# Kernel tuning notes

Hardware: AMD Instinct MI355X
Metric: run time of the kernel (lower is better)

Reference implementation:

```python
import jax, jax.numpy as jnp
import numpy as np

B, TQ, TK, DK, DV = 64, 1024, 1024, 64, 64


def setup_inputs() -> dict:
    key = jax.random.key(0)
    kq, kk, kv, km = jax.random.split(key, 4)
    q = jax.random.normal(kq, (B, TQ, DK), dtype=jnp.float32)
    k = jax.random.normal(kk, (B, TK, DK), dtype=jnp.float32)
    v = jax.random.normal(kv, (B, TK, DV), dtype=jnp.float32)
    mask = jax.random.randint(km, (B, TQ, TK), 0, 2).astype(jnp.int32)
    return {"q": q, "k": k, "v": v, "mask": mask}


def reference(q, k, v, mask):
    # attn = q @ k^T / sqrt(d_k)   -> [B, TQ, TK]
    temper = jnp.sqrt(jnp.asarray(q.shape[-1], dtype=jnp.float32))
    attn = jnp.einsum('bqd,bkd->bqk', q, k) / temper
    # mask-add: -1e9 where mask == 0
    mmask = -1e9 * (1.0 - mask.astype(jnp.float32))
    attn = attn + mmask
    attn = jax.nn.softmax(attn, axis=-1)
    # dropout rate is 0.0 -> identity
    out = jnp.einsum('bqk,bkd->bqd', attn, v)
    return (out, attn)
```

## Files before the change

### kernel.cpp

```cpp
#include <hip/hip_runtime.h>
#include <hip/hip_bf16.h>


#define B_   64
#define TQ_  1024
#define TK_  1024
#define DD   64

typedef short short8 __attribute__((ext_vector_type(8)));
typedef float f32x4 __attribute__((ext_vector_type(4)));

#define PSTR 264
#define VSTR 40
#define PWAVE (16 * PSTR)
#define VWAVE (64 * VSTR)

__device__ __forceinline__ unsigned cvt2(float a, float b) {
    __hip_bfloat162 h = __float22bfloat162_rn(make_float2(a, b));
    unsigned u; __builtin_memcpy(&u, &h, 4); return u;
}
__device__ __forceinline__ short cvt1(float a) {
    __hip_bfloat16 h = __float2bfloat16(a);
    short s; __builtin_memcpy(&s, &h, 2); return s;
}

union Frag { short8 s; unsigned u[4]; };

__global__ __launch_bounds__(256, 3) void attn_mfma_kernel(
    const float* __restrict__ qg, const float* __restrict__ kg,
    const float* __restrict__ vg, const int* __restrict__ maskg,
    float* __restrict__ outg, float* __restrict__ attng)
{
    __shared__ __align__(16) short p_lds[4 * PWAVE];
    __shared__ __align__(16) short vt_lds[4 * VWAVE];

    const int t    = threadIdx.x;
    const int wave = t >> 6, lane = t & 63;
    const int quad = lane >> 4, n16 = lane & 15;
    const int b    = blockIdx.y;
    const int q0   = blockIdx.x * 16;
    const int kbase = wave * 256;

    short* pw = p_lds + wave * PWAVE;
    short* vw = vt_lds + wave * VWAVE;
    float* redmax = (float*)vt_lds;
    float* redsum = (float*)vt_lds + 64;

    Frag aq[2];
    {
        const float* qp = qg + ((size_t)(b * TQ_ + q0 + n16)) * DD + quad * 8;
        #pragma unroll
        for (int f = 0; f < 2; ++f) {
            float4 x = *(const float4*)(qp + f * 32);
            float4 y = *(const float4*)(qp + f * 32 + 4);
            aq[f].u[0] = cvt2(x.x, x.y); aq[f].u[1] = cvt2(x.z, x.w);
            aq[f].u[2] = cvt2(y.x, y.y); aq[f].u[3] = cvt2(y.z, y.w);
        }
    }

    float s_reg[64];

    const float* kbp = kg + (size_t)b * TK_ * DD;
    const int*   mbp = maskg + ((size_t)(b * TQ_ + q0 + quad * 4)) * TK_ + kbase + n16;
    #pragma unroll
    for (int kt = 0; kt < 16; ++kt) {
        const int key0 = kbase + kt * 16;
        const float* kp = kbp + (size_t)(key0 + n16) * DD + quad * 8;
        Frag bk[2];
        #pragma unroll
        for (int f = 0; f < 2; ++f) {
            float4 x = *(const float4*)(kp + f * 32);
            float4 y = *(const float4*)(kp + f * 32 + 4);
            bk[f].u[0] = cvt2(x.x, x.y); bk[f].u[1] = cvt2(x.z, x.w);
            bk[f].u[2] = cvt2(y.x, y.y); bk[f].u[3] = cvt2(y.z, y.w);
        }
        f32x4 acc = {0.f, 0.f, 0.f, 0.f};
        acc = __builtin_amdgcn_mfma_f32_16x16x32_bf16(aq[0].s, bk[0].s, acc, 0, 0, 0);
        acc = __builtin_amdgcn_mfma_f32_16x16x32_bf16(aq[1].s, bk[1].s, acc, 0, 0, 0);
        #pragma unroll
        for (int r = 0; r < 4; ++r) {
            const int m = mbp[(size_t)r * TK_ + kt * 16];
            s_reg[kt * 4 + r] = acc[r] * 0.125f + (m ? 0.f : -1e9f);
        }
    }

    float rmax[4];
    #pragma unroll
    for (int r = 0; r < 4; ++r) {
        float m = s_reg[r];
        #pragma unroll
        for (int kt = 1; kt < 16; ++kt) m = fmaxf(m, s_reg[kt * 4 + r]);
        #pragma unroll
        for (int off = 8; off > 0; off >>= 1) m = fmaxf(m, __shfl_xor(m, off));
        rmax[r] = m;
    }
    if (n16 == 0) {
        #pragma unroll
        for (int r = 0; r < 4; ++r) redmax[wave * 16 + quad * 4 + r] = rmax[r];
    }
    __syncthreads();
    float gmax[4];
    #pragma unroll
    for (int r = 0; r < 4; ++r) {
        const int row = quad * 4 + r;
        gmax[r] = fmaxf(fmaxf(redmax[row], redmax[16 + row]),
                        fmaxf(redmax[32 + row], redmax[48 + row]));
    }
    float lsum[4] = {0.f, 0.f, 0.f, 0.f};
    #pragma unroll
    for (int kt = 0; kt < 16; ++kt) {
        #pragma unroll
        for (int r = 0; r < 4; ++r) {
            const float p = __expf(s_reg[kt * 4 + r] - gmax[r]);
            s_reg[kt * 4 + r] = p;
            lsum[r] += p;
        }
    }
    #pragma unroll
    for (int r = 0; r < 4; ++r) {
        #pragma unroll
        for (int off = 8; off > 0; off >>= 1) lsum[r] += __shfl_xor(lsum[r], off);
    }
    if (n16 == 0) {
        #pragma unroll
        for (int r = 0; r < 4; ++r) redsum[wave * 16 + quad * 4 + r] = lsum[r];
    }
    __syncthreads();
    float inv[4];
    #pragma unroll
    for (int r = 0; r < 4; ++r) {
        const int row = quad * 4 + r;
        inv[r] = 1.f / (redsum[row] + redsum[16 + row] + redsum[32 + row] + redsum[48 + row]);
    }
    __syncthreads();

    float* abp = attng + ((size_t)(b * TQ_ + q0 + quad * 4)) * TK_ + kbase + n16;
    #pragma unroll
    for (int kt = 0; kt < 16; ++kt) {
        #pragma unroll
        for (int r = 0; r < 4; ++r) {
            const float pv = s_reg[kt * 4 + r] * inv[r];
            abp[(size_t)r * TK_ + kt * 16] = pv;
            pw[(quad * 4 + r) * PSTR + kt * 16 + n16] = cvt1(pv);
        }
    }

    f32x4 oacc[4];
    #pragma unroll
    for (int dg = 0; dg < 4; ++dg) oacc[dg] = (f32x4){0.f, 0.f, 0.f, 0.f};

    const float* vbp = vg + (size_t)b * TK_ * DD;
    #pragma unroll 1
    for (int c = 0; c < 8; ++c) {
        const int ck0 = kbase + c * 32;
        #pragma unroll
        for (int i = 0; i < 16; ++i) {
            const float v0 = vbp[(size_t)(ck0 + 2 * i) * DD + lane];
            const float v1 = vbp[(size_t)(ck0 + 2 * i + 1) * DD + lane];
            *(unsigned*)(vw + lane * VSTR + 2 * i) = cvt2(v0, v1);
        }
        Frag pf;
        pf.s = *(const short8*)(pw + n16 * PSTR + c * 32 + quad * 8);
        #pragma unroll
        for (int dg = 0; dg < 4; ++dg) {
            Frag vf;
            vf.s = *(const short8*)(vw + (dg * 16 + n16) * VSTR + quad * 8);
            oacc[dg] = __builtin_amdgcn_mfma_f32_16x16x32_bf16(pf.s, vf.s, oacc[dg], 0, 0, 0);
        }
    }

    float* ow = (float*)pw;
    #pragma unroll
    for (int dg = 0; dg < 4; ++dg) {
        #pragma unroll
        for (int r = 0; r < 4; ++r)
            ow[(quad * 4 + r) * 68 + dg * 16 + n16] = oacc[dg][r];
    }
    __syncthreads();
    {
        const int row = t >> 4;
        const int col = (t & 15) * 4;
        const float* p0 = (const float*)p_lds;
        float4 o = make_float4(0.f, 0.f, 0.f, 0.f);
        #pragma unroll
        for (int w = 0; w < 4; ++w) {
            const float4 x = *(const float4*)(p0 + w * (PWAVE / 2) + row * 68 + col);
            o.x += x.x; o.y += x.y; o.z += x.z; o.w += x.w;
        }
        *(float4*)(outg + ((size_t)(b * TQ_ + q0 + row)) * DD + col) = o;
    }
}

extern "C" void kernel_launch(void* const* d_in, const int* in_sizes, int n_in,
                              void* d_out, int out_size, void* d_ws, size_t ws_size,
                              hipStream_t stream) {
    const float* q    = (const float*)d_in[0];
    const float* k    = (const float*)d_in[1];
    const float* v    = (const float*)d_in[2];
    const int*   mask = (const int*)d_in[3];

    float* out  = (float*)d_out;
    float* attn = out + (size_t)B_ * TQ_ * DD;

    dim3 grid(TQ_ / 16, B_);
    attn_mfma_kernel<<<grid, 256, 0, stream>>>(q, k, v, mask, out, attn);
}
```

Before: 628.8 us.

## Merge softmax reductions into one barrier and load V fragments directly from global

Each wave now computes its local row max and exp-sum, and the cross-wave combine rescales the partial sums, so two of the three block barriers go away. The V transpose through LDS is removed: each lane gathers its eight strided V elements straight from global memory and packs them into the MFMA operand. Dropping the V LDS buffer frees shared memory, and launch bounds are raised to target four blocks per CU. The trade-off is extra exp calls, uncoalesced strided global loads for V, and more register pressure from fully unrolling the V loop under a tighter occupancy target.

```diff
diff --git a/kernel.cpp b/kernel.cpp
--- a/kernel.cpp
+++ b/kernel.cpp
@@ -11,9 +11,7 @@
 typedef float f32x4 __attribute__((ext_vector_type(4)));
 
 #define PSTR 264
-#define VSTR 40
 #define PWAVE (16 * PSTR)
-#define VWAVE (64 * VSTR)
 
 __device__ __forceinline__ unsigned cvt2(float a, float b) {
     __hip_bfloat162 h = __float22bfloat162_rn(make_float2(a, b));
@@ -26,13 +24,14 @@
 
 union Frag { short8 s; unsigned u[4]; };
 
-__global__ __launch_bounds__(256, 3) void attn_mfma_kernel(
+__global__ __launch_bounds__(256, 4) void attn_mfma_kernel(
     const float* __restrict__ qg, const float* __restrict__ kg,
     const float* __restrict__ vg, const int* __restrict__ maskg,
     float* __restrict__ outg, float* __restrict__ attng)
 {
     __shared__ __align__(16) short p_lds[4 * PWAVE];
-    __shared__ __align__(16) short vt_lds[4 * VWAVE];
+    __shared__ float redm[4][16];
+    __shared__ float reds[4][16];
 
     const int t    = threadIdx.x;
     const int wave = t >> 6, lane = t & 63;
@@ -42,9 +41,6 @@
     const int kbase = wave * 256;
 
     short* pw = p_lds + wave * PWAVE;
-    short* vw = vt_lds + wave * VWAVE;
-    float* redmax = (float*)vt_lds;
-    float* redsum = (float*)vt_lds + 64;
 
     Frag aq[2];
     {
@@ -64,8 +60,7 @@
     const int*   mbp = maskg + ((size_t)(b * TQ_ + q0 + quad * 4)) * TK_ + kbase + n16;
     #pragma unroll
     for (int kt = 0; kt < 16; ++kt) {
-        const int key0 = kbase + kt * 16;
-        const float* kp = kbp + (size_t)(key0 + n16) * DD + quad * 8;
+        const float* kp = kbp + (size_t)(kbase + kt * 16 + n16) * DD + quad * 8;
         Frag bk[2];
         #pragma unroll
         for (int f = 0; f < 2; ++f) {
@@ -84,7 +79,7 @@
         }
     }
 
-    float rmax[4];
+    float lmax[4], lsum[4];
     #pragma unroll
     for (int r = 0; r < 4; ++r) {
         float m = s_reg[r];
@@ -92,26 +87,15 @@
         for (int kt = 1; kt < 16; ++kt) m = fmaxf(m, s_reg[kt * 4 + r]);
         #pragma unroll
         for (int off = 8; off > 0; off >>= 1) m = fmaxf(m, __shfl_xor(m, off));
-        rmax[r] = m;
+        lmax[r] = m;
     }
-    if (n16 == 0) {
-        #pragma unroll
-        for (int r = 0; r < 4; ++r) redmax[wave * 16 + quad * 4 + r] = rmax[r];
-    }
-    __syncthreads();
-    float gmax[4];
     #pragma unroll
-    for (int r = 0; r < 4; ++r) {
-        const int row = quad * 4 + r;
-        gmax[r] = fmaxf(fmaxf(redmax[row], redmax[16 + row]),
-                        fmaxf(redmax[32 + row], redmax[48 + row]));
-    }
-    float lsum[4] = {0.f, 0.f, 0.f, 0.f};
+    for (int r = 0; r < 4; ++r) lsum[r] = 0.f;
     #pragma unroll
     for (int kt = 0; kt < 16; ++kt) {
         #pragma unroll
         for (int r = 0; r < 4; ++r) {
-            const float p = __expf(s_reg[kt * 4 + r] - gmax[r]);
+            const float p = __expf(s_reg[kt * 4 + r] - lmax[r]);
             s_reg[kt * 4 + r] = p;
             lsum[r] += p;
         }
@@ -123,23 +107,32 @@
     }
     if (n16 == 0) {
         #pragma unroll
-        for (int r = 0; r < 4; ++r) redsum[wave * 16 + quad * 4 + r] = lsum[r];
+        for (int r = 0; r < 4; ++r) {
+            redm[wave][quad * 4 + r] = lmax[r];
+            reds[wave][quad * 4 + r] = lsum[r];
+        }
     }
     __syncthreads();
-    float inv[4];
+    float fscale[4];
     #pragma unroll
     for (int r = 0; r < 4; ++r) {
         const int row = quad * 4 + r;
-        inv[r] = 1.f / (redsum[row] + redsum[16 + row] + redsum[32 + row] + redsum[48 + row]);
+        const float m0 = redm[0][row], m1 = redm[1][row];
+        const float m2 = redm[2][row], m3 = redm[3][row];
+        const float gmax = fmaxf(fmaxf(m0, m1), fmaxf(m2, m3));
+        const float gsum = reds[0][row] * __expf(m0 - gmax)
+                         + reds[1][row] * __expf(m1 - gmax)
+                         + reds[2][row] * __expf(m2 - gmax)
+                         + reds[3][row] * __expf(m3 - gmax);
+        fscale[r] = __expf(lmax[r] - gmax) / gsum;
     }
-    __syncthreads();
 
     float* abp = attng + ((size_t)(b * TQ_ + q0 + quad * 4)) * TK_ + kbase + n16;
     #pragma unroll
     for (int kt = 0; kt < 16; ++kt) {
         #pragma unroll
         for (int r = 0; r < 4; ++r) {
-            const float pv = s_reg[kt * 4 + r] * inv[r];
+            const float pv = s_reg[kt * 4 + r] * fscale[r];
             abp[(size_t)r * TK_ + kt * 16] = pv;
             pw[(quad * 4 + r) * PSTR + kt * 16 + n16] = cvt1(pv);
         }
@@ -150,21 +143,20 @@
     for (int dg = 0; dg < 4; ++dg) oacc[dg] = (f32x4){0.f, 0.f, 0.f, 0.f};
 
     const float* vbp = vg + (size_t)b * TK_ * DD;
-    #pragma unroll 1
+    #pragma unroll
     for (int c = 0; c < 8; ++c) {
-        const int ck0 = kbase + c * 32;
-        #pragma unroll
-        for (int i = 0; i < 16; ++i) {
-            const float v0 = vbp[(size_t)(ck0 + 2 * i) * DD + lane];
-            const float v1 = vbp[(size_t)(ck0 + 2 * i + 1) * DD + lane];
-            *(unsigned*)(vw + lane * VSTR + 2 * i) = cvt2(v0, v1);
-        }
+        const int k0 = kbase + c * 32 + quad * 8;
         Frag pf;
         pf.s = *(const short8*)(pw + n16 * PSTR + c * 32 + quad * 8);
         #pragma unroll
         for (int dg = 0; dg < 4; ++dg) {
+            const float* vp = vbp + (size_t)k0 * DD + dg * 16 + n16;
+            float e[8];
+            #pragma unroll
+            for (int j = 0; j < 8; ++j) e[j] = vp[j * DD];
             Frag vf;
-            vf.s = *(const short8*)(vw + (dg * 16 + n16) * VSTR + quad * 8);
+            vf.u[0] = cvt2(e[0], e[1]); vf.u[1] = cvt2(e[2], e[3]);
+            vf.u[2] = cvt2(e[4], e[5]); vf.u[3] = cvt2(e[6], e[7]);
             oacc[dg] = __builtin_amdgcn_mfma_f32_16x16x32_bf16(pf.s, vf.s, oacc[dg], 0, 0, 0);
         }
     }
```

After: 657.2 us. +4.5%, slower.
